# Kernel tuning notes

Measured on AMD Instinct MI355X. Metric: run time of the kernel, lower is better.

Reference implementation:

```python
import jax, jax.numpy as jnp
import numpy as np
from jax import lax

# db4 reconstruction filters (pywt rec_lo / rec_hi), L = 8
DB4_REC_LO = np.array([0.23037781330885523, 0.7148465705525415, 0.6308807679295904,
                       -0.02798376941698385, -0.18703481171888114, 0.030841381835986965,
                       0.032883011666982945, -0.010597401784997278], dtype=np.float32)
DB4_REC_HI = np.array([-0.010597401784997278, -0.032883011666982945, 0.030841381835986965,
                       0.18703481171888114, -0.02798376941698385, -0.6308807679295904,
                       0.7148465705525415, -0.23037781330885523], dtype=np.float32)


def _conv_t1_last(x, w):
    """Transposed conv along last axis, stride 2, torch conv_transpose semantics.
    out[2i + k] += x[i] * w[k]; output length = 2n + L - 2."""
    shp = x.shape
    n = shp[-1]
    L = w.shape[0]
    x2 = x.reshape(-1, 1, n)                     # (B, 1, n)
    k = w[::-1].reshape(1, 1, L)                 # flip -> true convolution
    y = lax.conv_general_dilated(x2, k, window_strides=(1,),
                                 padding=[(L - 1, L - 1)], lhs_dilation=(2,))
    return y.reshape(shp[:-1] + (2 * n + L - 2,))


def _sfb1d(lo, hi, g0, g1, axis):
    """1D synthesis filter bank along `axis` with periodic (overlap-add) boundary."""
    lo = jnp.moveaxis(lo, axis, -1)
    hi = jnp.moveaxis(hi, axis, -1)
    n = lo.shape[-1]
    N = 2 * n
    L = g0.shape[0]
    y = _conv_t1_last(lo, g0) + _conv_t1_last(hi, g1)
    if y.shape[-1] > N:  # overlap-add wrap: y[:L-2] += y[N:N+L-2], then truncate
        y = y[..., :N].at[..., :L - 2].add(y[..., N:N + L - 2])
    y = jnp.roll(y, 1 - L // 2, axis=-1)
    return jnp.moveaxis(y, -1, axis)


def _sfb3d(y, g0, g1):
    # deinterleave 8 subbands from channel dim (stride-8 slicing, as in torch code)
    y0, y1, y2, y3 = y[:, 0::8], y[:, 1::8], y[:, 2::8], y[:, 3::8]
    y4, y5, y6, y7 = y[:, 4::8], y[:, 5::8], y[:, 6::8], y[:, 7::8]
    t0 = _sfb1d(y0, y1, g0, g1, 2)
    t1 = _sfb1d(y2, y3, g0, g1, 2)
    t2 = _sfb1d(y4, y5, g0, g1, 2)
    t3 = _sfb1d(y6, y7, g0, g1, 2)
    u0 = _sfb1d(t0, t1, g0, g1, 3)
    u1 = _sfb1d(t2, t3, g0, g1, 3)
    return _sfb1d(u0, u1, g0, g1, 4)


def setup_inputs() -> dict:
    key = jax.random.key(0)
    k1, k2, k3 = jax.random.split(key, 3)
    yl = jax.random.normal(k1, (4, 1, 64, 64, 64), dtype=jnp.float32)
    yh1 = jax.random.normal(k2, (4, 7, 128, 128, 128), dtype=jnp.float32)
    yh2 = jax.random.normal(k3, (4, 7, 64, 64, 64), dtype=jnp.float32)
    g0 = jnp.asarray(DB4_REC_LO)
    g1 = jnp.asarray(DB4_REC_HI)
    return {"yl": yl, "yh1": yh1, "yh2": yh2, "g0": g0, "g1": g1}


def reference(yl, yh1, yh2, g0, g1):
    ll = yl
    for h in (yh2, yh1):  # coarsest level first (yh[::-1] in torch)
        for d in (2, 3, 4):  # crop ll to match h if odd-length issue
            if ll.shape[d] > h.shape[d]:
                ll = lax.slice_in_dim(ll, 0, h.shape[d], axis=d)
        y_all = jnp.concatenate([ll, h], axis=1)
        ll = _sfb3d(y_all, g0, g1)
    return ll
```

## Files before the change

kernel.cpp:

```cpp
#include <hip/hip_runtime.h>

typedef float f32x4 __attribute__((ext_vector_type(4)));

#define G00 0.23037781330885523f
#define G01 0.7148465705525415f
#define G02 0.6308807679295904f
#define G03 -0.02798376941698385f
#define G04 -0.18703481171888114f
#define G05 0.030841381835986965f
#define G06 0.032883011666982945f
#define G07 -0.010597401784997278f

#define G10 -0.010597401784997278f
#define G11 -0.032883011666982945f
#define G12 0.030841381835986965f
#define G13 0.18703481171888114f
#define G14 -0.02798376941698385f
#define G15 -0.6308807679295904f
#define G16 0.7148465705525415f
#define G17 -0.23037781330885523f

template<int LOGN, bool NT>
__device__ __forceinline__ void phaseBC(f32x4* smem, float* __restrict__ out,
                                        int b, int d, int tile, int tid)
{
    constexpr int N = 1 << LOGN;
    constexpr int N4 = N / 4;
    constexpr int LOGN4 = LOGN - 2;
    constexpr int BELEMS = 2 * 32 * N4;
    constexpr int BITER  = BELEMS / 512;

    f32x4 ureg[BITER];
    #pragma unroll
    for (int it = 0; it < BITER; ++it) {
        int e = it * 512 + tid;
        int w4   = e & (N4 - 1);
        int rest = e >> LOGN4;
        int hl   = rest & 31;
        int qq   = rest >> 5;
        int ml = hl >> 1, pp = hl & 1;
        int ro = ml + pp + 3;
        float b0c = pp ? G00 : G01, b1c = pp ? G02 : G03;
        float b2c = pp ? G04 : G05, b3c = pp ? G06 : G07;
        float d0c = pp ? G10 : G11, d1c = pp ? G12 : G13;
        float d2c = pp ? G14 : G15, d3c = pp ? G16 : G17;
        int s0 = 2 * qq, s1 = s0 + 1;
        ureg[it] = b0c * smem[(s0 * 20 + ro    ) * N4 + w4]
                 + b1c * smem[(s0 * 20 + ro - 1) * N4 + w4]
                 + b2c * smem[(s0 * 20 + ro - 2) * N4 + w4]
                 + b3c * smem[(s0 * 20 + ro - 3) * N4 + w4]
                 + d0c * smem[(s1 * 20 + ro    ) * N4 + w4]
                 + d1c * smem[(s1 * 20 + ro - 1) * N4 + w4]
                 + d2c * smem[(s1 * 20 + ro - 2) * N4 + w4]
                 + d3c * smem[(s1 * 20 + ro - 3) * N4 + w4];
    }
    __syncthreads();
    #pragma unroll
    for (int it = 0; it < BITER; ++it) {
        smem[it * 512 + tid] = ureg[it];
    }
    __syncthreads();

    const float* ulf = (const float*)smem;
    float* orow_base = out + (((size_t)b * (2 * N) + d) * (2 * N) + (size_t)32 * tile) * (2 * N);
    for (int e = tid; e < 32 * (N / 2); e += 512) {
        int mw2 = e & (N / 2 - 1);
        int hl  = e >> (LOGN - 1);
        int mw  = mw2 * 2;
        const float* u0 = ulf + (size_t)hl * N;
        const float* u1 = ulf + (size_t)(32 + hl) * N;
        int mm2 = (mw - 2) & (N - 1), mm1 = (mw - 1) & (N - 1);
        int mp1 = (mw + 1) & (N - 1), mp2 = (mw + 2) & (N - 1), mp3 = (mw + 3) & (N - 1);
        float u0m2 = u0[mm2], u0m1 = u0[mm1], u00 = u0[mw];
        float u0p1 = u0[mp1], u0p2 = u0[mp2], u0p3 = u0[mp3];
        float u1m2 = u1[mm2], u1m1 = u1[mm1], u10 = u1[mw];
        float u1p1 = u1[mp1], u1p2 = u1[mp2], u1p3 = u1[mp3];
        f32x4 o;
        o.x = G01*u0p1 + G03*u00  + G05*u0m1 + G07*u0m2
            + G11*u1p1 + G13*u10  + G15*u1m1 + G17*u1m2;
        o.y = G00*u0p2 + G02*u0p1 + G04*u00  + G06*u0m1
            + G10*u1p2 + G12*u1p1 + G14*u10  + G16*u1m1;
        o.z = G01*u0p2 + G03*u0p1 + G05*u00  + G07*u0m1
            + G11*u1p2 + G13*u1p1 + G15*u10  + G17*u1m1;
        o.w = G00*u0p3 + G02*u0p2 + G04*u0p1 + G06*u00
            + G10*u1p3 + G12*u1p2 + G14*u1p1 + G16*u10;
        f32x4* dst = (f32x4*)(orow_base + (size_t)hl * (2 * N)) + mw2;
        if (NT) __builtin_nontemporal_store(o, dst);
        else    *dst = o;
    }
}

template<int LOGN, bool NT>
__global__ __launch_bounds__(512) void idwt3_fused2_k(
    const float* __restrict__ ll, const float* __restrict__ yh,
    float* __restrict__ out, int b0)
{
    constexpr int N = 1 << LOGN;
    constexpr int N4 = N / 4;
    constexpr int LOGN4 = LOGN - 2;
    constexpr int NN = N * N;
    constexpr size_t V = (size_t)N * N * N;
    constexpr int AELEMS = 4 * 20 * N4;
    constexpr int AITER  = (AELEMS + 511) / 512;

    __shared__ f32x4 smem[AELEMS];

    const int tid  = threadIdx.x;
    const int tile = blockIdx.x;
    const int mD   = blockIdx.y;
    const int b    = b0 + (int)blockIdx.z;

    const size_t q0 = (size_t)((mD - 2 + N) & (N - 1)) * NN;
    const size_t q1 = (size_t)((mD - 1 + N) & (N - 1)) * NN;
    const size_t q2 = (size_t)( mD                    ) * NN;
    const size_t q3 = (size_t)((mD + 1) & (N - 1)) * NN;
    const size_t q4 = (size_t)((mD + 2) & (N - 1)) * NN;

    const int h0in = 16 * tile - 2;
    const float* llb = ll + (size_t)b * V;
    const float* yb  = yh + (size_t)b * 7 * V;

    f32x4 treg[AITER];
    #pragma unroll
    for (int it = 0; it < AITER; ++it) {
        int e = it * 512 + tid;
        if (AELEMS % 512 != 0 && e >= AELEMS) continue;
        int w4 = e & (N4 - 1);
        int x  = e >> LOGN4;
        int pr = x / 20;
        int r  = x - 20 * pr;
        int hr = h0in + r;
        if (hr < 0) hr += N;
        if (hr >= N) hr -= N;
        const float* lo_base = (pr == 0) ? llb : (yb + (size_t)(2 * pr - 1) * V);
        const float* hi_base = yb + (size_t)(2 * pr) * V;
        int off = hr * N + w4 * 4;
        const float* lp = lo_base + off;
        const float* hp = hi_base + off;
        f32x4 Lm2 = *(const f32x4*)(lp + q0);
        f32x4 Lm1 = *(const f32x4*)(lp + q1);
        f32x4 L0c = *(const f32x4*)(lp + q2);
        f32x4 Lp1 = *(const f32x4*)(lp + q3);
        f32x4 Lp2 = *(const f32x4*)(lp + q4);
        f32x4 Hm2 = *(const f32x4*)(hp + q0);
        f32x4 Hm1 = *(const f32x4*)(hp + q1);
        f32x4 H0c = *(const f32x4*)(hp + q2);
        f32x4 Hp1 = *(const f32x4*)(hp + q3);
        f32x4 Hp2 = *(const f32x4*)(hp + q4);
        smem[e] = G01*Lp1 + G03*L0c + G05*Lm1 + G07*Lm2
                + G11*Hp1 + G13*H0c + G15*Hm1 + G17*Hm2;
        treg[it] = G00*Lp2 + G02*Lp1 + G04*L0c + G06*Lm1
                 + G10*Hp2 + G12*Hp1 + G14*H0c + G16*Hm1;
    }
    __syncthreads();

    phaseBC<LOGN, NT>(smem, out, b, 2 * mD, tile, tid);
    __syncthreads();

    #pragma unroll
    for (int it = 0; it < AITER; ++it) {
        int e = it * 512 + tid;
        if (AELEMS % 512 != 0 && e >= AELEMS) continue;
        smem[e] = treg[it];
    }
    __syncthreads();

    phaseBC<LOGN, NT>(smem, out, b, 2 * mD + 1, tile, tid);
}

__device__ __forceinline__ void phaseBC_l2(f32x4* smem, float* __restrict__ out,
                                           int b, int d, int tile, int tid)
{
    {
        const int w4 = tid & 31;
        const int qq = (tid >> 5) & 1;
        const int s  = tid >> 6;
        const f32x4* t0 = smem + ((2 * qq) * 20 + 2 * s) * 32 + w4;
        const f32x4* t1 = t0 + 20 * 32;
        f32x4 r0 = t0[0],   r1 = t0[32],  r2 = t0[64];
        f32x4 r3 = t0[96],  r4 = t0[128], r5 = t0[160];
        f32x4 e0 = t1[0],   e1 = t1[32],  e2 = t1[64];
        f32x4 e3 = t1[96],  e4 = t1[128], e5 = t1[160];
        f32x4 u0r = G01*r3 + G03*r2 + G05*r1 + G07*r0
                  + G11*e3 + G13*e2 + G15*e1 + G17*e0;
        f32x4 u1r = G00*r4 + G02*r3 + G04*r2 + G06*r1
                  + G10*e4 + G12*e3 + G14*e2 + G16*e1;
        f32x4 u2r = G01*r4 + G03*r3 + G05*r2 + G07*r1
                  + G11*e4 + G13*e3 + G15*e2 + G17*e1;
        f32x4 u3r = G00*r5 + G02*r4 + G04*r3 + G06*r2
                  + G10*e5 + G12*e4 + G14*e3 + G16*e2;
        __syncthreads();
        f32x4* ub = smem + ((qq * 32 + 4 * s) * 33 + w4);
        ub[0]  = u0r;
        ub[33] = u1r;
        ub[66] = u2r;
        ub[99] = u3r;
    }
    __syncthreads();

    float* orow_base = out + (((size_t)b * 256 + d) * 256 + (size_t)32 * tile) * 256;
    #pragma unroll
    for (int it = 0; it < 4; ++it) {
        int e  = it * 512 + tid;
        int ow = e & 63;
        int hl = e >> 6;
        int odd = ow & 1;
        int i0 = ((2 * ow - 2) & 127) >> 2;
        int i1 = ((2 * ow + 3) & 127) >> 2;
        const f32x4* u0r = smem + (size_t)hl * 33;
        const f32x4* u1r = smem + (size_t)(32 + hl) * 33;
        f32x4 P  = u0r[i0], Q  = u0r[i1];
        f32x4 Pp = u1r[i0], Qp = u1r[i1];
        float w0 = odd ? P[0]  : P[2],  w1 = odd ? P[1]  : P[3];
        float w2 = odd ? P[2]  : Q[0],  w3 = odd ? P[3]  : Q[1];
        float w4 = odd ? Q[0]  : Q[2],  w5 = odd ? Q[1]  : Q[3];
        float x0 = odd ? Pp[0] : Pp[2], x1 = odd ? Pp[1] : Pp[3];
        float x2 = odd ? Pp[2] : Qp[0], x3 = odd ? Pp[3] : Qp[1];
        float x4 = odd ? Qp[0] : Qp[2], x5 = odd ? Qp[1] : Qp[3];
        f32x4 o;
        o[0] = G01*w3 + G03*w2 + G05*w1 + G07*w0
             + G11*x3 + G13*x2 + G15*x1 + G17*x0;
        o[1] = G00*w4 + G02*w3 + G04*w2 + G06*w1
             + G10*x4 + G12*x3 + G14*x2 + G16*x1;
        o[2] = G01*w4 + G03*w3 + G05*w2 + G07*w1
             + G11*x4 + G13*x3 + G15*x2 + G17*x1;
        o[3] = G00*w5 + G02*w4 + G04*w3 + G06*w2
             + G10*x5 + G12*x4 + G14*x3 + G16*x2;
        f32x4* dst = (f32x4*)(orow_base + (size_t)hl * 256) + ow;
        __builtin_nontemporal_store(o, dst);
    }
}

#define AISSUE(P, k) { \
    int x_ = (k) * 16 + xr; int pr_ = x_ / 20; int r_ = x_ - 20 * pr_; \
    int hr_ = h0in + r_; if (hr_ < 0) hr_ += 128; if (hr_ >= 128) hr_ -= 128; \
    const float* lo_ = (pr_ == 0) ? llb : (yb + (size_t)(2 * pr_ - 1) * V); \
    const float* hi_ = yb + (size_t)(2 * pr_) * V; \
    const float* lp_ = lo_ + hr_ * 128 + w4c * 4; \
    const float* hp_ = hi_ + hr_ * 128 + w4c * 4; \
    P##0 = *(const f32x4*)(lp_ + q0); P##1 = *(const f32x4*)(lp_ + q1); \
    P##2 = *(const f32x4*)(lp_ + q2); P##3 = *(const f32x4*)(lp_ + q3); \
    P##4 = *(const f32x4*)(lp_ + q4); \
    P##5 = *(const f32x4*)(hp_ + q0); P##6 = *(const f32x4*)(hp_ + q1); \
    P##7 = *(const f32x4*)(hp_ + q2); P##8 = *(const f32x4*)(hp_ + q3); \
    P##9 = *(const f32x4*)(hp_ + q4); }

#define ACONS(P, k) { \
    smem[(k) * 512 + tid] = G01*P##3 + G03*P##2 + G05*P##1 + G07*P##0 \
                          + G11*P##8 + G13*P##7 + G15*P##6 + G17*P##5; \
    treg[k]               = G00*P##4 + G02*P##3 + G04*P##2 + G06*P##1 \
                          + G10*P##9 + G12*P##8 + G14*P##7 + G16*P##6; }

__global__ __launch_bounds__(512) void idwt3_l2_k(
    const float* __restrict__ ll, const float* __restrict__ yh,
    float* __restrict__ out)
{
    constexpr int N = 128;
    constexpr int NN = N * N;
    constexpr size_t V = (size_t)N * N * N;

    __shared__ f32x4 smem[2560];

    const int tid  = threadIdx.x;
    const int tile = blockIdx.x;
    const int mD   = blockIdx.y;
    const int b    = blockIdx.z;

    const size_t q0 = (size_t)((mD - 2 + N) & (N - 1)) * NN;
    const size_t q1 = (size_t)((mD - 1 + N) & (N - 1)) * NN;
    const size_t q2 = (size_t)( mD                    ) * NN;
    const size_t q3 = (size_t)((mD + 1) & (N - 1)) * NN;
    const size_t q4 = (size_t)((mD + 2) & (N - 1)) * NN;

    const int h0in = 16 * tile - 2;
    const float* llb = ll + (size_t)b * V;
    const float* yb  = yh + (size_t)b * 7 * V;
    const int xr  = tid >> 5;
    const int w4c = tid & 31;

    f32x4 treg[5];
    f32x4 A0, A1, A2, A3, A4, A5, A6, A7, A8, A9;
    f32x4 B0, B1, B2, B3, B4, B5, B6, B7, B8, B9;

    AISSUE(A, 0);
    AISSUE(B, 1);
    ACONS(A, 0);
    AISSUE(A, 2);
    ACONS(B, 1);
    AISSUE(B, 3);
    ACONS(A, 2);
    AISSUE(A, 4);
    ACONS(B, 3);
    ACONS(A, 4);
    __syncthreads();

    phaseBC_l2(smem, out, b, 2 * mD, tile, tid);
    __syncthreads();

    #pragma unroll
    for (int it = 0; it < 5; ++it) smem[it * 512 + tid] = treg[it];
    __syncthreads();

    phaseBC_l2(smem, out, b, 2 * mD + 1, tile, tid);
}


extern "C" void kernel_launch(void* const* d_in, const int* in_sizes, int n_in,
                              void* d_out, int out_size, void* d_ws, size_t ws_size,
                              hipStream_t stream)
{
    const float* yl  = (const float*)d_in[0];
    const float* yh1 = (const float*)d_in[1];
    const float* yh2 = (const float*)d_in[2];
    float* outf = (float*)d_out;
    float* ll1  = (float*)d_ws;

    idwt3_fused2_k<6, false><<<dim3(4, 64, 4), 512, 0, stream>>>(yl, yh2, ll1, 0);

    idwt3_l2_k<<<dim3(8, 128, 4), 512, 0, stream>>>(ll1, yh1, outf);
}
```

Measured before the change: 177.1 us.

## Process two input depth slices per block to reuse overlapping D-axis loads

Each block of the level-2 kernel now covers two consecutive input depth planes (four output depth planes) instead of one. It loads six depth taps instead of five for both lo and hi, so the load per output plane drops from five taps to three. Grid depth is halved and each block runs four smem phases with three register-held temporaries. This cuts redundant global reads, but holding 15 f32x4 temporaries raises register pressure, and removing the explicit A/B load double-buffering may reduce memory-level parallelism.

```diff
diff --git a/kernel.cpp b/kernel.cpp
--- a/kernel.cpp
+++ b/kernel.cpp
@@ -231,27 +231,33 @@
     }
 }
 
-#define AISSUE(P, k) { \
+#define ABATCH(k) { \
     int x_ = (k) * 16 + xr; int pr_ = x_ / 20; int r_ = x_ - 20 * pr_; \
     int hr_ = h0in + r_; if (hr_ < 0) hr_ += 128; if (hr_ >= 128) hr_ -= 128; \
     const float* lo_ = (pr_ == 0) ? llb : (yb + (size_t)(2 * pr_ - 1) * V); \
     const float* hi_ = yb + (size_t)(2 * pr_) * V; \
     const float* lp_ = lo_ + hr_ * 128 + w4c * 4; \
     const float* hp_ = hi_ + hr_ * 128 + w4c * 4; \
-    P##0 = *(const f32x4*)(lp_ + q0); P##1 = *(const f32x4*)(lp_ + q1); \
-    P##2 = *(const f32x4*)(lp_ + q2); P##3 = *(const f32x4*)(lp_ + q3); \
-    P##4 = *(const f32x4*)(lp_ + q4); \
-    P##5 = *(const f32x4*)(hp_ + q0); P##6 = *(const f32x4*)(hp_ + q1); \
-    P##7 = *(const f32x4*)(hp_ + q2); P##8 = *(const f32x4*)(hp_ + q3); \
-    P##9 = *(const f32x4*)(hp_ + q4); }
-
-#define ACONS(P, k) { \
-    smem[(k) * 512 + tid] = G01*P##3 + G03*P##2 + G05*P##1 + G07*P##0 \
-                          + G11*P##8 + G13*P##7 + G15*P##6 + G17*P##5; \
-    treg[k]               = G00*P##4 + G02*P##3 + G04*P##2 + G06*P##1 \
-                          + G10*P##9 + G12*P##8 + G14*P##7 + G16*P##6; }
-
-__global__ __launch_bounds__(512) void idwt3_l2_k(
+    f32x4 L0 = *(const f32x4*)(lp_ + q0), L1 = *(const f32x4*)(lp_ + q1); \
+    f32x4 L2 = *(const f32x4*)(lp_ + q2), L3 = *(const f32x4*)(lp_ + q3); \
+    f32x4 L4 = *(const f32x4*)(lp_ + q4), L5 = *(const f32x4*)(lp_ + q5); \
+    f32x4 H0 = *(const f32x4*)(hp_ + q0), H1 = *(const f32x4*)(hp_ + q1); \
+    f32x4 H2 = *(const f32x4*)(hp_ + q2), H3 = *(const f32x4*)(hp_ + q3); \
+    f32x4 H4 = *(const f32x4*)(hp_ + q4), H5 = *(const f32x4*)(hp_ + q5); \
+    smem[(k) * 512 + tid] = G01*L3 + G03*L2 + G05*L1 + G07*L0 \
+                          + G11*H3 + G13*H2 + G15*H1 + G17*H0; \
+    tA1[k] = G00*L4 + G02*L3 + G04*L2 + G06*L1 \
+           + G10*H4 + G12*H3 + G14*H2 + G16*H1; \
+    tB0[k] = G01*L4 + G03*L3 + G05*L2 + G07*L1 \
+           + G11*H4 + G13*H3 + G15*H2 + G17*H1; \
+    tB1[k] = G00*L5 + G02*L4 + G04*L3 + G06*L2 \
+           + G10*H5 + G12*H4 + G14*H3 + G16*H2; }
+
+#define TSWAP(tarr) { \
+    _Pragma("unroll") \
+    for (int it_ = 0; it_ < 5; ++it_) smem[it_ * 512 + tid] = (tarr)[it_]; }
+
+__global__ __launch_bounds__(512) void idwt3_l2q_k(
     const float* __restrict__ ll, const float* __restrict__ yh,
     float* __restrict__ out)
 {
@@ -263,14 +269,15 @@
 
     const int tid  = threadIdx.x;
     const int tile = blockIdx.x;
-    const int mD   = blockIdx.y;
+    const int g    = blockIdx.y;
     const int b    = blockIdx.z;
 
-    const size_t q0 = (size_t)((mD - 2 + N) & (N - 1)) * NN;
-    const size_t q1 = (size_t)((mD - 1 + N) & (N - 1)) * NN;
-    const size_t q2 = (size_t)( mD                    ) * NN;
-    const size_t q3 = (size_t)((mD + 1) & (N - 1)) * NN;
-    const size_t q4 = (size_t)((mD + 2) & (N - 1)) * NN;
+    const size_t q0 = (size_t)((2 * g - 2 + N) & (N - 1)) * NN;
+    const size_t q1 = (size_t)((2 * g - 1 + N) & (N - 1)) * NN;
+    const size_t q2 = (size_t)( 2 * g                    ) * NN;
+    const size_t q3 = (size_t)((2 * g + 1) & (N - 1)) * NN;
+    const size_t q4 = (size_t)((2 * g + 2) & (N - 1)) * NN;
+    const size_t q5 = (size_t)((2 * g + 3) & (N - 1)) * NN;
 
     const int h0in = 16 * tile - 2;
     const float* llb = ll + (size_t)b * V;
@@ -278,30 +285,24 @@
     const int xr  = tid >> 5;
     const int w4c = tid & 31;
 
-    f32x4 treg[5];
-    f32x4 A0, A1, A2, A3, A4, A5, A6, A7, A8, A9;
-    f32x4 B0, B1, B2, B3, B4, B5, B6, B7, B8, B9;
-
-    AISSUE(A, 0);
-    AISSUE(B, 1);
-    ACONS(A, 0);
-    AISSUE(A, 2);
-    ACONS(B, 1);
-    AISSUE(B, 3);
-    ACONS(A, 2);
-    AISSUE(A, 4);
-    ACONS(B, 3);
-    ACONS(A, 4);
-    __syncthreads();
-
-    phaseBC_l2(smem, out, b, 2 * mD, tile, tid);
-    __syncthreads();
-
-    #pragma unroll
-    for (int it = 0; it < 5; ++it) smem[it * 512 + tid] = treg[it];
-    __syncthreads();
-
-    phaseBC_l2(smem, out, b, 2 * mD + 1, tile, tid);
+    f32x4 tA1[5], tB0[5], tB1[5];
+
+    ABATCH(0); ABATCH(1); ABATCH(2); ABATCH(3); ABATCH(4);
+    __syncthreads();
+
+    phaseBC_l2(smem, out, b, 4 * g + 0, tile, tid);
+    __syncthreads();
+    TSWAP(tA1);
+    __syncthreads();
+    phaseBC_l2(smem, out, b, 4 * g + 1, tile, tid);
+    __syncthreads();
+    TSWAP(tB0);
+    __syncthreads();
+    phaseBC_l2(smem, out, b, 4 * g + 2, tile, tid);
+    __syncthreads();
+    TSWAP(tB1);
+    __syncthreads();
+    phaseBC_l2(smem, out, b, 4 * g + 3, tile, tid);
 }
 
 
@@ -317,5 +318,5 @@
 
     idwt3_fused2_k<6, false><<<dim3(4, 64, 4), 512, 0, stream>>>(yl, yh2, ll1, 0);
 
-    idwt3_l2_k<<<dim3(8, 128, 4), 512, 0, stream>>>(ll1, yh1, outf);
-}
+    idwt3_l2q_k<<<dim3(8, 64, 4), 512, 0, stream>>>(ll1, yh1, outf);
+}
```

After: 161.2 us. -9.0%, faster.
